# Kernel optimization log

Hardware: AMD Instinct MI355X
Metric: run time of the kernel (lower is better)

## Reference

```python
import jax, jax.numpy as jnp
import numpy as np

PADDING = 1024
STRIDE = 1


def setup_inputs() -> dict:
    key = jax.random.key(0)
    k1, k2, k3 = jax.random.split(key, 3)
    signal = jax.random.normal(k1, (32, 128, 8192), dtype=jnp.float32)
    weight = jax.random.normal(k2, (128, 128, 2048), dtype=jnp.float32) * 0.02
    bias = jax.random.normal(k3, (128,), dtype=jnp.float32)
    return {"signal": signal, "weight": weight, "bias": bias}


def reference(signal, weight, bias):
    # 1D FFT convolution: pad -> rfft -> complex matmul (a * conj(b)) -> irfft -> crop -> bias.
    sig = jnp.pad(signal, ((0, 0), (0, 0), (PADDING, PADDING)))
    L = sig.shape[-1]          # padded signal length (10240)
    K = weight.shape[-1]       # kernel size (2048)

    sig_fr = jnp.fft.rfft(sig, axis=-1)            # [B, Cin, F] complex64
    ker_fr = jnp.fft.rfft(weight, n=L, axis=-1)    # [Cout, Cin, F] (zero-padded kernel)

    # torch code computes (aR*bR + aI*bI, aI*bR - aR*bI) == a * conj(b)
    out_fr = jnp.einsum('bif,oif->bof', sig_fr, jnp.conj(ker_fr))

    out = jnp.fft.irfft(out_fr, n=L, axis=-1)      # [B, Cout, L]
    out = out[:, :, ::STRIDE]
    out = out[:, :, : (L - K) // STRIDE + 1]       # valid-conv crop -> length 8193
    return out + bias[None, :, None]
```

## Files before the change

### kernel.cpp

```cpp
#include <hip/hip_runtime.h>
#include <hip/hip_fp16.h>


#define THREADS 256
#define CTHREADS 512
#define FP 2056
#define NFB 514

struct alignas(16) H2x4 { __half2 h[4]; };

typedef _Float16 f16x8 __attribute__((ext_vector_type(8)));
typedef float f32x4 __attribute__((ext_vector_type(4)));

__device__ __forceinline__ float2 f2(float x, float y){ return make_float2(x, y); }
__device__ __forceinline__ __half2 pack2(float x, float y){ return __floats2half2_rn(x, y); }
__device__ __forceinline__ float2 unpack2(__half2 h){
  return make_float2(__low2float(h), __high2float(h));
}
__device__ __forceinline__ float2 cmul(float2 a, float2 b){
  return make_float2(a.x*b.x - a.y*b.y, a.x*b.y + a.y*b.x);
}

__device__ float2* fft2048(float2* A, float2* B, int tid, float sign){
  float2* src = A; float2* dst = B;
  #pragma unroll 1
  for (int st = 0; st < 5; ++st){
    const int twos = 2*st;
    const int L = 1 << twos;
    const float crev = sign * 0.25f / (float)L;
    __syncthreads();
    #pragma unroll
    for (int r = 0; r < 2; ++r){
      int j = tid + (r << 8);
      int p = j & (L - 1);
      int q = j >> twos;
      float rev = crev * (float)p;
      float sa = __builtin_amdgcn_sinf(rev);
      float ca = __builtin_amdgcn_cosf(rev);
      float2 wa = f2(ca, sa);
      float2 w  = f2(ca*ca - sa*sa, 2.0f*ca*sa);
      float2 x0 = src[j];
      float2 x1 = src[j + 512];
      float2 x2 = src[j + 1024];
      float2 x3 = src[j + 1536];
      float2 t2 = cmul(w, x2);
      float2 t3 = cmul(w, x3);
      float2 u0 = f2(x0.x + t2.x, x0.y + t2.y);
      float2 u1 = f2(x0.x - t2.x, x0.y - t2.y);
      float2 u2 = f2(x1.x + t3.x, x1.y + t3.y);
      float2 u3 = f2(x1.x - t3.x, x1.y - t3.y);
      float2 v2 = cmul(wa, u2);
      float2 v3 = cmul(wa, u3);
      float2 iv3 = f2(-sign * v3.y, sign * v3.x);
      int ob = (q << (twos + 2)) + p;
      dst[ob]       = f2(u0.x + v2.x,  u0.y + v2.y);
      dst[ob + L]   = f2(u1.x + iv3.x, u1.y + iv3.y);
      dst[ob + 2*L] = f2(u0.x - v2.x,  u0.y - v2.y);
      dst[ob + 3*L] = f2(u1.x - iv3.x, u1.y - iv3.y);
    }
    float2* t = src; src = dst; dst = t;
  }
  {
    const float crev = sign * 0.5f / 1024.0f;
    __syncthreads();
    #pragma unroll
    for (int r = 0; r < 4; ++r){
      int j = tid + (r << 8);
      float rev = crev * (float)j;
      float sw = __builtin_amdgcn_sinf(rev);
      float cw = __builtin_amdgcn_cosf(rev);
      float2 a = src[j];
      float2 b = src[j + 1024];
      float tr = b.x*cw - b.y*sw;
      float ti = b.x*sw + b.y*cw;
      dst[j]        = f2(a.x + tr, a.y + ti);
      dst[j + 1024] = f2(a.x - tr, a.y - ti);
    }
    float2* t = src; src = dst; dst = t;
  }
  __syncthreads();
  return src;
}

__device__ void unpack_store(const float2* Z, __half2* out, int tid){
  for (int k = tid; k < 2048; k += THREADS){
    float2 zk = Z[k];
    float2 zm = Z[(2048 - k) & 2047];
    float ar =  0.5f*(zk.x + zm.x);
    float ai =  0.5f*(zk.y - zm.y);
    float br =  0.5f*(zk.y + zm.y);
    float bi = -0.5f*(zk.x - zm.x);
    float rev = -(float)k * (1.0f/4096.0f);
    float sw = __builtin_amdgcn_sinf(rev);
    float cw = __builtin_amdgcn_cosf(rev);
    out[k] = pack2(ar + cw*br - sw*bi, ai + cw*bi + sw*br);
  }
  if (tid == 0){
    float2 z0 = Z[0];
    out[2048] = pack2(z0.x - z0.y, 0.0f);
  }
  if (tid >= 1 && tid < 8) out[2048 + tid] = pack2(0.0f, 0.0f);
}

__global__ __launch_bounds__(THREADS) void kfft_w(const float* __restrict__ w,
                                                  __half2* __restrict__ Wc, int o_base){
  __shared__ float2 A[2048]; __shared__ float2 B[2048];
  int lr = blockIdx.x;
  int grow = (o_base + (lr >> 7)) * 128 + (lr & 127);
  const float2* wv = (const float2*)(w + (size_t)grow * 2048);
  for (int n = threadIdx.x; n < 2048; n += THREADS)
    A[n] = (n < 1024) ? wv[n] : f2(0.f, 0.f);
  float2* Z = fft2048(A, B, threadIdx.x, -1.0f);
  unpack_store(Z, Wc + (size_t)lr * FP, threadIdx.x);
}

__global__ __launch_bounds__(THREADS) void kfft_s(const float* __restrict__ sig,
                                                  __half2* __restrict__ Xc, int bb_base){
  __shared__ float2 A[2048]; __shared__ float2 B[2048];
  int lr = blockIdx.x;
  int bb = bb_base + (lr >> 7), i = lr & 127;
  int b = bb >> 2, blk = bb & 3;
  const float2* sv = (const float2*)(sig + (size_t)(b*128 + i) * 8192);
  for (int n = threadIdx.x; n < 2048; n += THREADS){
    int q = n + blk*1024 - 512;
    A[n] = (q >= 0 && q < 4096) ? sv[q] : f2(0.f, 0.f);
  }
  float2* Z = fft2048(A, B, threadIdx.x, -1.0f);
  unpack_store(Z, Xc + (size_t)lr * FP, threadIdx.x);
}

__global__ __launch_bounds__(CTHREADS, 4) void kceinsum(
    const __half2* __restrict__ Xc, const __half2* __restrict__ Wc,
    __half2* __restrict__ Yc, int nbbBlk, int OC)
{
  __shared__ char sb[32768] __attribute__((aligned(16)));
  const int total = gridDim.x;
  const int nt = total / NFB;
  int wg = blockIdx.x;
  int w = ((total & 7) == 0) ? ((wg & 7) * (total >> 3) + (wg >> 3)) : wg;
  const int x = w % nt;
  const int y = w / nt;
  const int bb0 = (x % nbbBlk) * 64;
  const int o0  = (x / nbbBlk) * 64;
  const int f0  = y * 4;

  const int tid = threadIdx.x;
  const int wave = tid >> 6, lane = tid & 63;
  const int wm = wave >> 2;
  const int wn = wave & 3;
  const int l15 = lane & 15, l4 = lane >> 4;

  const int r0  = (tid >> 3) & 63;
  const int ip2 = tid & 7;
  const __half2* pA = Xc + ((size_t)(bb0 + r0) * 128 + ip2 * 2) * FP + f0;
  const __half2* pB = Wc + ((size_t)(o0 + r0) * 128 + ip2 * 2) * FP + f0;

  const f32x4 zv = {0.f, 0.f, 0.f, 0.f};
  f32x4 accR[2][4], accI[2][4];
  #pragma unroll
  for (int mt = 0; mt < 2; ++mt)
    #pragma unroll
    for (int c = 0; c < 4; ++c){ accR[mt][c] = zv; accI[mt][c] = zv; }

  uint4 va0 = *(const uint4*)pA;
  uint4 va1 = *(const uint4*)(pA + FP);
  uint4 vb0 = *(const uint4*)pB;
  uint4 vb1 = *(const uint4*)(pB + FP);

  const unsigned wswz = ((unsigned)(r0 & 7)) << 4;

  #pragma unroll 1
  for (int ic = 0; ic < 8; ++ic){
    __syncthreads();
    {
      const unsigned* a0 = (const unsigned*)&va0;
      const unsigned* a1 = (const unsigned*)&va1;
      const unsigned* b0 = (const unsigned*)&vb0;
      const unsigned* b1 = (const unsigned*)&vb1;
      #pragma unroll
      for (int c = 0; c < 4; ++c){
        unsigned off = ((((unsigned)r0 << 7) + ((unsigned)(c & 1) << 6) +
                         ((unsigned)ip2 << 3)) ^ wswz) + (((unsigned)(c >> 1)) << 13);
        *(uint2*)(sb + off)         = make_uint2(a0[c], a1[c]);
        *(uint2*)(sb + 16384 + off) = make_uint2(b0[c], b1[c]);
      }
    }
    if (ic < 7){
      const __half2* qA = pA + (size_t)(ic + 1) * 16 * FP;
      const __half2* qB = pB + (size_t)(ic + 1) * 16 * FP;
      va0 = *(const uint4*)qA;
      va1 = *(const uint4*)(qA + FP);
      vb0 = *(const uint4*)qB;
      vb1 = *(const uint4*)(qB + FP);
    }
    __syncthreads();
    #pragma unroll
    for (int c = 0; c < 4; ++c){
      const unsigned cb = (((unsigned)(c >> 1)) << 13);
      const unsigned cf = ((unsigned)(c & 1)) << 6;
      f16x8 af[2];
      #pragma unroll
      for (int mt = 0; mt < 2; ++mt){
        unsigned row = (unsigned)(wm*32 + mt*16 + l15);
        unsigned off = ((row << 7) + cf + ((unsigned)l4 << 4)) ^ ((row & 7) << 4);
        af[mt] = *(const f16x8*)(sb + cb + off);
      }
      unsigned orow = (unsigned)(wn*16 + l15);
      unsigned offb = ((orow << 7) + cf + ((unsigned)l4 << 4)) ^ ((orow & 7) << 4);
      f16x8 bf = *(const f16x8*)(sb + 16384 + cb + offb);
      union { f16x8 v; unsigned u[4]; } sB, dB;
      sB.v = bf;
      #pragma unroll
      for (int j = 0; j < 4; ++j)
        dB.u[j] = ((sB.u[j] >> 16) | (sB.u[j] << 16)) ^ 0x00008000u;
      #pragma unroll
      for (int mt = 0; mt < 2; ++mt){
        accR[mt][c] = __builtin_amdgcn_mfma_f32_16x16x32_f16(af[mt], bf,   accR[mt][c], 0, 0, 0);
        accI[mt][c] = __builtin_amdgcn_mfma_f32_16x16x32_f16(af[mt], dB.v, accI[mt][c], 0, 0, 0);
      }
    }
  }
  const int olg = o0 + wn*16 + l15;
  #pragma unroll
  for (int mt = 0; mt < 2; ++mt)
    #pragma unroll
    for (int r = 0; r < 4; ++r){
      int bbl = bb0 + wm*32 + mt*16 + l4*4 + r;
      H2x4 hv;
      #pragma unroll
      for (int c = 0; c < 4; ++c) hv.h[c] = pack2(accR[mt][c][r], accI[mt][c][r]);
      *(H2x4*)(Yc + ((size_t)bbl * NFB + y) * OC * 4 + (size_t)olg * 4) = hv;
    }
}

template<int TO>
__global__ __launch_bounds__(THREADS) void keinsum(const __half2* __restrict__ Xc,
                                                   const __half2* __restrict__ Wc,
                                                   __half2* __restrict__ Yc, int OC){
  constexpr int OGN = TO/4;
  constexpr int BB_PER = TO/8;
  __shared__ float2 Xs[16*64];
  __shared__ float2 Ws[TO*67];
  const int bb0 = blockIdx.x * 16;
  const int f0  = blockIdx.y * 8;
  const int o0  = blockIdx.z * TO;
  const int tid = threadIdx.x;
  const int f_id = tid & 7;
  const int g  = tid >> 3;
  const int og = g & (OGN - 1);
  const int bg = g / OGN;
  float2 acc[BB_PER][4];
  #pragma unroll
  for (int a_ = 0; a_ < BB_PER; ++a_)
    #pragma unroll
    for (int b_ = 0; b_ < 4; ++b_) acc[a_][b_] = f2(0.f, 0.f);

  for (int ic = 0; ic < 16; ++ic){
    __syncthreads();
    #pragma unroll
    for (int l = 0; l < TO/16; ++l){
      int u = l*THREADS + tid;
      int o = u >> 4, ii = (u >> 1) & 7, c = u & 1;
      H2x4 v = *(const H2x4*)(Wc + (size_t)((o0 + o)*128 + ic*8 + ii)*FP + f0 + c*4);
      #pragma unroll
      for (int j = 0; j < 4; ++j) Ws[o*67 + ii*8 + c*4 + j] = unpack2(v.h[j]);
    }
    {
      int u = tid;
      int bbi = u >> 4, ii = (u >> 1) & 7, c = u & 1;
      H2x4 v = *(const H2x4*)(Xc + (size_t)((bb0 + bbi)*128 + ic*8 + ii)*FP + f0 + c*4);
      #pragma unroll
      for (int j = 0; j < 4; ++j) Xs[bbi*64 + ii*8 + c*4 + j] = unpack2(v.h[j]);
    }
    __syncthreads();
    #pragma unroll
    for (int ii = 0; ii < 8; ++ii){
      float2 xv[BB_PER], wv[4];
      #pragma unroll
      for (int bj = 0; bj < BB_PER; ++bj) xv[bj] = Xs[(bg*BB_PER + bj)*64 + ii*8 + f_id];
      #pragma unroll
      for (int oj = 0; oj < 4; ++oj) wv[oj] = Ws[(og*4 + oj)*67 + ii*8 + f_id];
      #pragma unroll
      for (int bj = 0; bj < BB_PER; ++bj)
        #pragma unroll
        for (int oj = 0; oj < 4; ++oj){
          acc[bj][oj].x += xv[bj].x*wv[oj].x + xv[bj].y*wv[oj].y;
          acc[bj][oj].y += xv[bj].y*wv[oj].x - xv[bj].x*wv[oj].y;
        }
    }
  }
  #pragma unroll
  for (int bj = 0; bj < BB_PER; ++bj)
    #pragma unroll
    for (int oj = 0; oj < 4; ++oj){
      int row = (bb0 + bg*BB_PER + bj)*OC + (o0 + og*4 + oj);
      Yc[(size_t)row*FP + f0 + f_id] = pack2(acc[bj][oj].x, acc[bj][oj].y);
    }
}

__global__ __launch_bounds__(THREADS) void kifft(const __half2* __restrict__ Yc,
                                                 const float* __restrict__ bias,
                                                 float* __restrict__ out,
                                                 int bb_base, int o_base, int oc_shift,
                                                 int newlay){
  __shared__ float2 A[2048]; __shared__ float2 B[2048];
  __shared__ float XMs;
  int lr = blockIdx.x;
  int OCm = (1 << oc_shift) - 1;
  int bbl = lr >> oc_shift, ol = lr & OCm;
  int bb = bb_base + bbl;
  int o  = o_base + ol;
  int b = bb >> 2, blk = bb & 3;
  int tid = threadIdx.x;
  if (newlay){
    const size_t ustr = (size_t)(OCm + 1) * 4;
    const __half2* Yb = Yc + (size_t)bbl * NFB * ustr + (size_t)ol * 4;
    #pragma unroll
    for (int l = 0; l < 2; ++l){
      int u = l*THREADS + tid;
      H2x4 v = *(const H2x4*)(Yb + (size_t)u * ustr);
      #pragma unroll
      for (int j = 0; j < 4; ++j) B[u*4 + j] = unpack2(v.h[j]);
    }
    if (tid == 0) XMs = __low2float(Yb[512 * ustr]);
  } else {
    const __half2* Y = Yc + (size_t)lr * FP;
    #pragma unroll
    for (int l = 0; l < 2; ++l){
      int u = l*THREADS + tid;
      H2x4 v = *(const H2x4*)(Y + u*4);
      #pragma unroll
      for (int j = 0; j < 4; ++j) B[u*4 + j] = unpack2(v.h[j]);
    }
    if (tid == 0) XMs = __low2float(Y[2048]);
  }
  __syncthreads();
  for (int k = tid; k < 2048; k += THREADS){
    float2 xk = B[k];
    float2 xm = (k == 0) ? f2(XMs, 0.f) : B[2048 - k];
    float ar = 0.5f*(xk.x + xm.x);
    float ai = 0.5f*(xk.y - xm.y);
    float dr = 0.5f*(xk.x - xm.x);
    float di = 0.5f*(xk.y + xm.y);
    float rev = (float)k * (1.0f/4096.0f);
    float sw = __builtin_amdgcn_sinf(rev);
    float cw = __builtin_amdgcn_cosf(rev);
    float br = dr*cw - di*sw;
    float bi = dr*sw + di*cw;
    A[k] = f2(ar - bi, ai + br);
  }
  float2* z = fft2048(A, B, tid, +1.0f);
  const float s = 1.0f/2048.0f;
  const float bv = bias[o];
  float* op = out + (size_t)(b*128 + o)*8193 + blk*2048;
  for (int n = tid; n < 2048; n += THREADS){
    if (n < 1024){
      op[2*n]     = z[n].x*s + bv;
      op[2*n + 1] = z[n].y*s + bv;
    } else if (n == 1024 && blk == 3){
      op[2048] = z[n].x*s + bv;
    }
  }
}

extern "C" void kernel_launch(void* const* d_in, const int* in_sizes, int n_in,
                              void* d_out, int out_size, void* d_ws, size_t ws_size,
                              hipStream_t stream){
  (void)in_sizes; (void)n_in; (void)out_size;
  const float* sig  = (const float*)d_in[0];
  const float* wgt  = (const float*)d_in[1];
  const float* bias = (const float*)d_in[2];
  float* out = (float*)d_out;
  const size_t rowb = (size_t)FP * sizeof(__half2);

  static const int modes[7][2] = {{128,128},{128,64},{128,32},{128,16},{64,16},{32,16},{16,16}};
  int OC = 0, BC = 0;
  for (int m = 0; m < 7; ++m){
    size_t need = ((size_t)modes[m][0]*128 + (size_t)modes[m][1]*128 +
                   (size_t)modes[m][1]*modes[m][0]) * rowb;
    if (need <= ws_size){ OC = modes[m][0]; BC = modes[m][1]; break; }
  }
  if (!OC) return;
  int ocs = 0; while ((1 << ocs) != OC) ++ocs;

  char* ws = (char*)d_ws;
  __half2* Wc = (__half2*)ws;
  __half2* Xc = (__half2*)(ws + (size_t)OC*128*rowb);
  __half2* Yc = (__half2*)(ws + ((size_t)OC*128 + (size_t)BC*128)*rowb);

  for (int ob = 0; ob < 128; ob += OC){
    hipLaunchKernelGGL(kfft_w, dim3(OC*128), dim3(THREADS), 0, stream, wgt, Wc, ob);
    for (int bbb = 0; bbb < 128; bbb += BC){
      hipLaunchKernelGGL(kfft_s, dim3(BC*128), dim3(THREADS), 0, stream, sig, Xc, bbb);
      int newlay = ((BC & 63) == 0 && (OC & 63) == 0) ? 1 : 0;
      if (newlay){
        int nbb = BC >> 6, no = OC >> 6;
        hipLaunchKernelGGL(kceinsum, dim3(nbb*no*NFB), dim3(CTHREADS), 0, stream,
                           Xc, Wc, Yc, nbb, OC);
      } else {
        dim3 ge(BC/16, FP/8, OC >= 64 ? OC/64 : 1);
        if (OC >= 64)
          hipLaunchKernelGGL(HIP_KERNEL_NAME(keinsum<64>), ge, dim3(THREADS), 0, stream, Xc, Wc, Yc, OC);
        else if (OC == 32)
          hipLaunchKernelGGL(HIP_KERNEL_NAME(keinsum<32>), ge, dim3(THREADS), 0, stream, Xc, Wc, Yc, OC);
        else
          hipLaunchKernelGGL(HIP_KERNEL_NAME(keinsum<16>), ge, dim3(THREADS), 0, stream, Xc, Wc, Yc, OC);
      }
      hipLaunchKernelGGL(kifft, dim3(BC*OC), dim3(THREADS), 0, stream, Yc, bias, out, bbb, ob, ocs, newlay);
    }
  }
}
```

Before: 856.6 us.

## Swizzle FFT shared-memory indices and double-buffer einsum global prefetch

```diff
diff --git a/kernel.cpp b/kernel.cpp
--- a/kernel.cpp
+++ b/kernel.cpp
@@ -6,6 +6,8 @@
 #define CTHREADS 512
 #define FP 2056
 #define NFB 514
+
+#define SWZ(i) (((i) ^ (((i) >> 4) & 15)))
 
 struct alignas(16) H2x4 { __half2 h[4]; };
 
@@ -39,10 +41,11 @@
       float ca = __builtin_amdgcn_cosf(rev);
       float2 wa = f2(ca, sa);
       float2 w  = f2(ca*ca - sa*sa, 2.0f*ca*sa);
-      float2 x0 = src[j];
-      float2 x1 = src[j + 512];
-      float2 x2 = src[j + 1024];
-      float2 x3 = src[j + 1536];
+      int js = SWZ(j);
+      float2 x0 = src[js];
+      float2 x1 = src[js + 512];
+      float2 x2 = src[js + 1024];
+      float2 x3 = src[js + 1536];
       float2 t2 = cmul(w, x2);
       float2 t3 = cmul(w, x3);
       float2 u0 = f2(x0.x + t2.x, x0.y + t2.y);
@@ -53,10 +56,10 @@
       float2 v3 = cmul(wa, u3);
       float2 iv3 = f2(-sign * v3.y, sign * v3.x);
       int ob = (q << (twos + 2)) + p;
-      dst[ob]       = f2(u0.x + v2.x,  u0.y + v2.y);
-      dst[ob + L]   = f2(u1.x + iv3.x, u1.y + iv3.y);
-      dst[ob + 2*L] = f2(u0.x - v2.x,  u0.y - v2.y);
-      dst[ob + 3*L] = f2(u1.x - iv3.x, u1.y - iv3.y);
+      dst[SWZ(ob)]       = f2(u0.x + v2.x,  u0.y + v2.y);
+      dst[SWZ(ob + L)]   = f2(u1.x + iv3.x, u1.y + iv3.y);
+      dst[SWZ(ob + 2*L)] = f2(u0.x - v2.x,  u0.y - v2.y);
+      dst[SWZ(ob + 3*L)] = f2(u1.x - iv3.x, u1.y - iv3.y);
     }
     float2* t = src; src = dst; dst = t;
   }
@@ -69,12 +72,13 @@
       float rev = crev * (float)j;
       float sw = __builtin_amdgcn_sinf(rev);
       float cw = __builtin_amdgcn_cosf(rev);
-      float2 a = src[j];
-      float2 b = src[j + 1024];
+      int js = SWZ(j);
+      float2 a = src[js];
+      float2 b = src[js + 1024];
       float tr = b.x*cw - b.y*sw;
       float ti = b.x*sw + b.y*cw;
-      dst[j]        = f2(a.x + tr, a.y + ti);
-      dst[j + 1024] = f2(a.x - tr, a.y - ti);
+      dst[js]        = f2(a.x + tr, a.y + ti);
+      dst[js + 1024] = f2(a.x - tr, a.y - ti);
     }
     float2* t = src; src = dst; dst = t;
   }
@@ -84,8 +88,8 @@
 
 __device__ void unpack_store(const float2* Z, __half2* out, int tid){
   for (int k = tid; k < 2048; k += THREADS){
-    float2 zk = Z[k];
-    float2 zm = Z[(2048 - k) & 2047];
+    float2 zk = Z[SWZ(k)];
+    float2 zm = Z[SWZ((2048 - k) & 2047)];
     float ar =  0.5f*(zk.x + zm.x);
     float ai =  0.5f*(zk.y - zm.y);
     float br =  0.5f*(zk.y + zm.y);
@@ -109,7 +113,7 @@
   int grow = (o_base + (lr >> 7)) * 128 + (lr & 127);
   const float2* wv = (const float2*)(w + (size_t)grow * 2048);
   for (int n = threadIdx.x; n < 2048; n += THREADS)
-    A[n] = (n < 1024) ? wv[n] : f2(0.f, 0.f);
+    A[SWZ(n)] = (n < 1024) ? wv[n] : f2(0.f, 0.f);
   float2* Z = fft2048(A, B, threadIdx.x, -1.0f);
   unpack_store(Z, Wc + (size_t)lr * FP, threadIdx.x);
 }
@@ -123,7 +127,7 @@
   const float2* sv = (const float2*)(sig + (size_t)(b*128 + i) * 8192);
   for (int n = threadIdx.x; n < 2048; n += THREADS){
     int q = n + blk*1024 - 512;
-    A[n] = (q >= 0 && q < 4096) ? sv[q] : f2(0.f, 0.f);
+    A[SWZ(n)] = (q >= 0 && q < 4096) ? sv[q] : f2(0.f, 0.f);
   }
   float2* Z = fft2048(A, B, threadIdx.x, -1.0f);
   unpack_store(Z, Xc + (size_t)lr * FP, threadIdx.x);
@@ -162,38 +166,25 @@
     #pragma unroll
     for (int c = 0; c < 4; ++c){ accR[mt][c] = zv; accI[mt][c] = zv; }
 
-  uint4 va0 = *(const uint4*)pA;
-  uint4 va1 = *(const uint4*)(pA + FP);
-  uint4 vb0 = *(const uint4*)pB;
-  uint4 vb1 = *(const uint4*)(pB + FP);
-
   const unsigned wswz = ((unsigned)(r0 & 7)) << 4;
-
-  #pragma unroll 1
-  for (int ic = 0; ic < 8; ++ic){
-    __syncthreads();
-    {
-      const unsigned* a0 = (const unsigned*)&va0;
-      const unsigned* a1 = (const unsigned*)&va1;
-      const unsigned* b0 = (const unsigned*)&vb0;
-      const unsigned* b1 = (const unsigned*)&vb1;
-      #pragma unroll
-      for (int c = 0; c < 4; ++c){
-        unsigned off = ((((unsigned)r0 << 7) + ((unsigned)(c & 1) << 6) +
-                         ((unsigned)ip2 << 3)) ^ wswz) + (((unsigned)(c >> 1)) << 13);
-        *(uint2*)(sb + off)         = make_uint2(a0[c], a1[c]);
-        *(uint2*)(sb + 16384 + off) = make_uint2(b0[c], b1[c]);
-      }
-    }
-    if (ic < 7){
-      const __half2* qA = pA + (size_t)(ic + 1) * 16 * FP;
-      const __half2* qB = pB + (size_t)(ic + 1) * 16 * FP;
-      va0 = *(const uint4*)qA;
-      va1 = *(const uint4*)(qA + FP);
-      vb0 = *(const uint4*)qB;
-      vb1 = *(const uint4*)(qB + FP);
-    }
-    __syncthreads();
+  unsigned offc[4];
+  #pragma unroll
+  for (int c = 0; c < 4; ++c)
+    offc[c] = ((((unsigned)r0 << 7) + ((unsigned)(c & 1) << 6) +
+                ((unsigned)ip2 << 3)) ^ wswz) + (((unsigned)(c >> 1)) << 13);
+
+  auto ldst = [&](const uint4& x0, const uint4& x1, const uint4& y0, const uint4& y1){
+    const unsigned* a0 = (const unsigned*)&x0;
+    const unsigned* a1 = (const unsigned*)&x1;
+    const unsigned* b0 = (const unsigned*)&y0;
+    const unsigned* b1 = (const unsigned*)&y1;
+    #pragma unroll
+    for (int c = 0; c < 4; ++c){
+      *(uint2*)(sb + offc[c])         = make_uint2(a0[c], a1[c]);
+      *(uint2*)(sb + 16384 + offc[c]) = make_uint2(b0[c], b1[c]);
+    }
+  };
+  auto comp = [&](){
     #pragma unroll
     for (int c = 0; c < 4; ++c){
       const unsigned cb = (((unsigned)(c >> 1)) << 13);
@@ -219,6 +210,43 @@
         accI[mt][c] = __builtin_amdgcn_mfma_f32_16x16x32_f16(af[mt], dB.v, accI[mt][c], 0, 0, 0);
       }
     }
+  };
+
+  uint4 xA0 = *(const uint4*)pA;
+  uint4 xA1 = *(const uint4*)(pA + FP);
+  uint4 yA0 = *(const uint4*)pB;
+  uint4 yA1 = *(const uint4*)(pB + FP);
+  uint4 xB0 = *(const uint4*)(pA + (size_t)16 * FP);
+  uint4 xB1 = *(const uint4*)(pA + (size_t)17 * FP);
+  uint4 yB0 = *(const uint4*)(pB + (size_t)16 * FP);
+  uint4 yB1 = *(const uint4*)(pB + (size_t)17 * FP);
+
+  #pragma unroll 1
+  for (int ic = 0; ic < 8; ic += 2){
+    __syncthreads();
+    ldst(xA0, xA1, yA0, yA1);
+    if (ic < 6){
+      const __half2* qA = pA + (size_t)(ic + 2) * 16 * FP;
+      const __half2* qB = pB + (size_t)(ic + 2) * 16 * FP;
+      xA0 = *(const uint4*)qA;
+      xA1 = *(const uint4*)(qA + FP);
+      yA0 = *(const uint4*)qB;
+      yA1 = *(const uint4*)(qB + FP);
+    }
+    __syncthreads();
+    comp();
+    __syncthreads();
+    ldst(xB0, xB1, yB0, yB1);
+    if (ic < 5){
+      const __half2* qA = pA + (size_t)(ic + 3) * 16 * FP;
+      const __half2* qB = pB + (size_t)(ic + 3) * 16 * FP;
+      xB0 = *(const uint4*)qA;
+      xB1 = *(const uint4*)(qA + FP);
+      yB0 = *(const uint4*)qB;
+      yB1 = *(const uint4*)(qB + FP);
+    }
+    __syncthreads();
+    comp();
   }
   const int olg = o0 + wn*16 + l15;
   #pragma unroll
@@ -320,7 +348,7 @@
       int u = l*THREADS + tid;
       H2x4 v = *(const H2x4*)(Yb + (size_t)u * ustr);
       #pragma unroll
-      for (int j = 0; j < 4; ++j) B[u*4 + j] = unpack2(v.h[j]);
+      for (int j = 0; j < 4; ++j) B[SWZ(u*4 + j)] = unpack2(v.h[j]);
     }
     if (tid == 0) XMs = __low2float(Yb[512 * ustr]);
   } else {
@@ -330,14 +358,14 @@
       int u = l*THREADS + tid;
       H2x4 v = *(const H2x4*)(Y + u*4);
       #pragma unroll
-      for (int j = 0; j < 4; ++j) B[u*4 + j] = unpack2(v.h[j]);
+      for (int j = 0; j < 4; ++j) B[SWZ(u*4 + j)] = unpack2(v.h[j]);
     }
     if (tid == 0) XMs = __low2float(Y[2048]);
   }
   __syncthreads();
   for (int k = tid; k < 2048; k += THREADS){
-    float2 xk = B[k];
-    float2 xm = (k == 0) ? f2(XMs, 0.f) : B[2048 - k];
+    float2 xk = B[SWZ(k)];
+    float2 xm = (k == 0) ? f2(XMs, 0.f) : B[SWZ(2048 - k)];
     float ar = 0.5f*(xk.x + xm.x);
     float ai = 0.5f*(xk.y - xm.y);
     float dr = 0.5f*(xk.x - xm.x);
@@ -347,18 +375,19 @@
     float cw = __builtin_amdgcn_cosf(rev);
     float br = dr*cw - di*sw;
     float bi = dr*sw + di*cw;
-    A[k] = f2(ar - bi, ai + br);
+    A[SWZ(k)] = f2(ar - bi, ai + br);
   }
   float2* z = fft2048(A, B, tid, +1.0f);
   const float s = 1.0f/2048.0f;
   const float bv = bias[o];
   float* op = out + (size_t)(b*128 + o)*8193 + blk*2048;
   for (int n = tid; n < 2048; n += THREADS){
+    float2 zn = z[SWZ(n)];
     if (n < 1024){
-      op[2*n]     = z[n].x*s + bv;
-      op[2*n + 1] = z[n].y*s + bv;
+      op[2*n]     = zn.x*s + bv;
+      op[2*n + 1] = zn.y*s + bv;
     } else if (n == 1024 && blk == 3){
-      op[2048] = z[n].x*s + bv;
+      op[2048] = zn.x*s + bv;
     }
   }
 }
```

Measured after the change: 871.7 us. Within noise of the previous version (+1.8%).
